# Kernel tuning notes

Measured on AMD Instinct MI355X. Metric: run time of the kernel, lower is better.

## Reference

```python
import jax, jax.numpy as jnp
import numpy as np

B, T, C, H, DH = 2, 2048, 768, 12, 64


def setup_inputs() -> dict:
    key = jax.random.key(0)
    k1, k2, k3 = jax.random.split(key, 3)
    x = jax.random.normal(k1, (B, T, C), dtype=jnp.float32)
    Wqkv = jax.random.normal(k2, (C, 3 * C), dtype=jnp.float32) * (C ** -0.5)
    Wout = jax.random.normal(k3, (C, C), dtype=jnp.float32) * (C ** -0.5)
    return {"x": x, "Wqkv": Wqkv, "Wout": Wout}


def reference(x, Wqkv, Wout):
    b, t, c = x.shape
    qkv = x @ Wqkv  # [B,T,3C]
    q, k, v = jnp.split(qkv, 3, axis=-1)
    # [B,T,C] -> [B,H,T,dh]
    q = q.reshape(b, t, H, DH).transpose(0, 2, 1, 3)
    k = k.reshape(b, t, H, DH).transpose(0, 2, 1, 3)
    v = v.reshape(b, t, H, DH).transpose(0, 2, 1, 3)
    scale = DH ** -0.5
    scores = jnp.einsum('bhqd,bhkd->bhqk', q, k) * scale  # [B,H,T,T]
    causal = jnp.tril(jnp.ones((t, t), dtype=bool))
    scores = jnp.where(causal, scores, -jnp.inf)
    weights = jax.nn.softmax(scores, axis=-1)
    # dropout p=0.0 -> identity
    out = jnp.einsum('bhqk,bhkd->bhqd', weights, v)  # [B,H,T,dh]
    out = out.transpose(0, 2, 1, 3).reshape(b, t, c)
    return out @ Wout
```

## Files before the change

kernel.cpp:

```cpp
#include <hip/hip_runtime.h>
#include <hip/hip_bf16.h>

#define Bn 2
#define Tn 2048
#define Cn 768
#define Hn 12
#define Dn 64
#define N3n 2304
#define Mn 4096

#define MASKVAL (-30000.f)
#define NITEMS 1152
#define DEFER_THR 64.f
#define L2E8 0.1803368801111204f

typedef unsigned short u16;
typedef __attribute__((ext_vector_type(8))) unsigned short ushort8_t;
typedef __attribute__((ext_vector_type(8))) short bf16x8;
typedef __attribute__((ext_vector_type(4))) float f32x4;
typedef __attribute__((ext_vector_type(2))) unsigned int uint2v;
typedef __attribute__((address_space(1))) unsigned int* gas1_t;
typedef __attribute__((address_space(3))) unsigned int* las3_t;

__device__ __forceinline__ float bf2f(u16 u) {
  union { unsigned int i; float f; } v; v.i = ((unsigned int)u) << 16; return v.f;
}
__device__ __forceinline__ u16 f2bf(float f) {
  union { float f; unsigned int i; } v; v.f = f;
  return (u16)((v.i + 0x7fffu + ((v.i >> 16) & 1u)) >> 16);
}

#define E(qt, s0, s1, ck) (((qt) << 24) | ((s0) << 16) | ((s1) << 8) | (ck))
__constant__ unsigned int SCHED[48] = {
    E(31, 0, 16, 0), E(31, 16, 32, 1), E(30, 0, 16, 0), E(15, 0, 16, 2),
    E(30, 16, 31, 1), E(29, 0, 15, 0), E(29, 15, 30, 1), E(28, 0, 15, 0), E(14, 0, 15, 2),
    E(28, 15, 29, 1), E(27, 0, 14, 0), E(27, 14, 28, 1), E(26, 0, 14, 0), E(13, 0, 14, 2),
    E(26, 14, 27, 1), E(25, 0, 13, 0), E(25, 13, 26, 1), E(24, 0, 13, 0), E(12, 0, 13, 2),
    E(24, 13, 25, 1), E(23, 0, 12, 0), E(23, 12, 24, 1), E(22, 0, 12, 0), E(11, 0, 12, 2),
    E(22, 12, 23, 1), E(21, 0, 11, 0), E(21, 11, 22, 1), E(20, 0, 11, 0), E(10, 0, 11, 2),
    E(20, 11, 21, 1), E(19, 0, 10, 0), E(19, 10, 20, 1), E(18, 0, 10, 0), E(9, 0, 10, 2),
    E(18, 10, 19, 1), E(17, 0, 9, 0), E(17, 9, 18, 1), E(16, 0, 9, 0), E(8, 0, 9, 2),
    E(16, 9, 17, 1), E(7, 0, 8, 2),
    E(6, 0, 7, 2), E(5, 0, 6, 2), E(4, 0, 5, 2), E(3, 0, 4, 2), E(2, 0, 3, 2),
    E(1, 0, 2, 2), E(0, 0, 1, 2)};

__global__ __launch_bounds__(256) void prep_kernel(const float* __restrict__ x,
                                                   const float* __restrict__ Wqkv,
                                                   const float* __restrict__ Wout,
                                                   u16* __restrict__ xb,
                                                   u16* __restrict__ WqkvT,
                                                   u16* __restrict__ WoutT,
                                                   int* __restrict__ counter) {
  __shared__ u16 t[32][33];
  const int bx = blockIdx.x;
  const int tid = threadIdx.x;
  if (bx < 3072) {
    if (bx == 0 && tid == 0) *counter = 0;
    const int i = (bx * 256 + tid) * 4;
    float4 v = *(const float4*)(x + i);
    ushort4 s;
    s.x = f2bf(v.x); s.y = f2bf(v.y); s.z = f2bf(v.z); s.w = f2bf(v.w);
    *(ushort4*)(xb + i) = s;
  } else {
    const int idx = bx - 3072;
    const int gx = idx % 96, gy = idx / 96;
    const bool isA = gx < (N3n / 32);
    const float* in = isA ? Wqkv : Wout;
    u16* out = isA ? WqkvT : WoutT;
    const int Cc = isA ? N3n : Cn;
    const int c0 = (isA ? gx : gx - N3n / 32) * 32;
    const int r0 = gy * 32;
    const int tx = tid & 31, ty = tid >> 5;
#pragma unroll
    for (int i = 0; i < 4; i++)
      t[ty * 4 + i][tx] = f2bf(in[(size_t)(r0 + ty * 4 + i) * Cc + c0 + tx]);
    __syncthreads();
#pragma unroll
    for (int i = 0; i < 4; i++)
      out[(size_t)(c0 + ty * 4 + i) * Cn + r0 + tx] = t[tx][ty * 4 + i];
  }
}

#define BK 64

template <int EPI>
__global__ __launch_bounds__(256) void mfma_gemm(const u16* __restrict__ A,
                                                 const u16* __restrict__ BT,
                                                 u16* __restrict__ Q,
                                                 u16* __restrict__ Kd,
                                                 u16* __restrict__ VT,
                                                 float* __restrict__ out) {
  __shared__ __align__(16) u16 Ash[128 * BK];
  __shared__ __align__(16) u16 Bsh[128 * BK];
  const int tid = threadIdx.x;
  const int wv = tid >> 6, lane = tid & 63;
  const int lo = lane & 15, quad = lane >> 4;
  const int wm = wv & 1, wn = wv >> 1;

  const int nwg = gridDim.x * gridDim.y;
  const int cpx = nwg >> 3;
  const int lid = blockIdx.y * gridDim.x + blockIdx.x;
  const int swz = (lid & 7) * cpx + (lid >> 3);
  const int n0 = (swz % gridDim.x) * 128;
  const int m0 = (swz / gridDim.x) * 128;

  const int srow = lane >> 3;
  const int scol = (lane & 7) << 3;

  f32x4 acc[4][4];
#pragma unroll
  for (int i = 0; i < 4; i++)
#pragma unroll
    for (int j = 0; j < 4; j++) acc[i][j] = f32x4{0.f, 0.f, 0.f, 0.f};

  for (int k0 = 0; k0 < Cn; k0 += BK) {
    __syncthreads();
#pragma unroll
    for (int c = 0; c < 4; c++) {
      const int rb = (wv << 5) + (c << 3);
      const int gr = rb + srow;
      __builtin_amdgcn_global_load_lds(
          (gas1_t)(A + (size_t)(m0 + gr) * Cn + k0 + scol),
          (las3_t)(&Ash[rb * BK]), 16, 0, 0);
      __builtin_amdgcn_global_load_lds(
          (gas1_t)(BT + (size_t)(n0 + gr) * Cn + k0 + scol),
          (las3_t)(&Bsh[rb * BK]), 16, 0, 0);
    }
    __syncthreads();

    bf16x8 af[4][2], bfr[4][2];
#pragma unroll
    for (int t = 0; t < 4; t++) {
#pragma unroll
      for (int s = 0; s < 2; s++) {
        af[t][s]  = *(const bf16x8*)&Ash[(wm * 64 + t * 16 + lo) * BK + s * 32 + (quad << 3)];
        bfr[t][s] = *(const bf16x8*)&Bsh[(wn * 64 + t * 16 + lo) * BK + s * 32 + (quad << 3)];
      }
    }
#pragma unroll
    for (int mt = 0; mt < 4; mt++)
#pragma unroll
      for (int nt = 0; nt < 4; nt++) {
        acc[mt][nt] = __builtin_amdgcn_mfma_f32_16x16x32_bf16(af[mt][0], bfr[nt][0],
                                                              acc[mt][nt], 0, 0, 0);
        acc[mt][nt] = __builtin_amdgcn_mfma_f32_16x16x32_bf16(af[mt][1], bfr[nt][1],
                                                              acc[mt][nt], 0, 0, 0);
      }
  }

  if (EPI == 0) {
    const int which = n0 / Cn;
    const int h = ((n0 % Cn) >> 6) + wn;
    const int bb = m0 >> 11;
    const int t_base = (m0 & (Tn - 1)) + wm * 64;
    if (which < 2) {
      u16* dst = ((which == 0) ? Q : Kd) + (size_t)(bb * Hn + h) * Tn * Dn;
#pragma unroll
      for (int mt = 0; mt < 4; mt++)
#pragma unroll
        for (int nt = 0; nt < 4; nt++)
#pragma unroll
          for (int r = 0; r < 4; r++) {
            const int t = t_base + mt * 16 + (quad << 2) + r;
            dst[(size_t)t * Dn + nt * 16 + lo] = f2bf(acc[mt][nt][r]);
          }
    } else {
      u16* dst = VT + (size_t)(bb * Hn + h) * Dn * Tn;
#pragma unroll
      for (int mt = 0; mt < 4; mt++)
#pragma unroll
        for (int nt = 0; nt < 4; nt++) {
          const int t = t_base + mt * 16 + (quad << 2);
          const int d = nt * 16 + lo;
          ushort4 st;
          st.x = f2bf(acc[mt][nt][0]); st.y = f2bf(acc[mt][nt][1]);
          st.z = f2bf(acc[mt][nt][2]); st.w = f2bf(acc[mt][nt][3]);
          *(ushort4*)&dst[(size_t)d * Tn + t] = st;
        }
    }
  } else {
#pragma unroll
    for (int mt = 0; mt < 4; mt++)
#pragma unroll
      for (int nt = 0; nt < 4; nt++)
#pragma unroll
        for (int r = 0; r < 4; r++) {
          const int m = m0 + wm * 64 + mt * 16 + (quad << 2) + r;
          out[(size_t)m * Cn + n0 + wn * 64 + nt * 16 + lo] = acc[mt][nt][r];
        }
  }
}

#define TILE_W (64 * 64)

__global__ __launch_bounds__(256) void attn_kernel(const u16* __restrict__ Q,
                                                   const u16* __restrict__ K,
                                                   const u16* __restrict__ VT,
                                                   u16* __restrict__ O,
                                                   int* __restrict__ counter,
                                                   float* __restrict__ po,
                                                   float* __restrict__ pm,
                                                   float* __restrict__ pl) {
  __shared__ __align__(16) u16 Ksh[2 * TILE_W];
  __shared__ __align__(16) u16 Vsh[2 * TILE_W];
  int* sip = (int*)&Ksh[TILE_W];

  const int tid = threadIdx.x;
  const int wv = tid >> 6, lane = tid & 63;
  const int lo = lane & 15, quad = lane >> 4;
  const int lo7 = lo & 7;
  const int ck0 = (quad ^ lo7) << 3;
  const int ck1 = ck0 ^ 32;
  const int sr = tid >> 3;
  const int sc = (tid & 7) << 3;
  const int scw = (((tid & 7) ^ (sr & 7)) << 3);
  const int t7 = tid & 7;
  const int vb0 = (((t7 & 6) ^ (sr & 7)) << 3) + ((t7 & 1) << 2);
  const int vb1 = ((((t7 & 6) | 1) ^ (sr & 7)) << 3) + ((t7 & 1) << 2);

  for (;;) {
    if (tid == 0) *sip = atomicAdd(counter, 1);
    __syncthreads();
    const int item = *sip;
    if (item >= NITEMS) return;

    const unsigned int e = SCHED[item / 24];
    const int qt = e >> 24, ck = e & 255;
    const int jstart = ((e >> 16) & 255) << 6;
    const int jend   = ((e >> 8) & 255) << 6;
    const int q0 = qt << 6;
    const int hb = item % 24;
    const int h = hb % 12, b = hb / 12;
    const size_t base = (size_t)(b * Hn + h) * Tn * Dn;
    const size_t vtb  = (size_t)(b * Hn + h) * Dn * Tn;

    const u16* qp = Q + base + (size_t)(q0 + (wv << 4) + lo) * Dn + (quad << 3);
    const bf16x8 aq0 = *(const bf16x8*)qp;
    const bf16x8 aq1 = *(const bf16x8*)(qp + 32);

    f32x4 o[4] = {f32x4{0,0,0,0}, f32x4{0,0,0,0}, f32x4{0,0,0,0}, f32x4{0,0,0,0}};
    float m1 = MASKVAL;
    float l1 = 0.f;

#pragma unroll
    for (int it = 0; it < 2; it++) {
      const int r = sr + it * 32;
      *(ushort8_t*)&Ksh[r * 64 + scw] =
          *(const ushort8_t*)(K + base + (size_t)(jstart + r) * Dn + sc);
      union { ushort8_t u; uint2v hh[2]; } vv;
      vv.u = *(const ushort8_t*)(VT + vtb + (size_t)r * Tn + jstart + sc);
      *(uint2v*)&Vsh[r * 64 + vb0] = vv.hh[0];
      *(uint2v*)&Vsh[r * 64 + vb1] = vv.hh[1];
    }
    __syncthreads();

    int cur = 0;
    const int qrel = (wv << 4) + lo;

    for (int j0 = jstart; j0 < jend; j0 += 64) {
      const bool hasnext = (j0 + 64 < jend);

      ushort8_t kr[2], vr[2];
      if (hasnext) {
#pragma unroll
        for (int it = 0; it < 2; it++) {
          const int r = sr + it * 32;
          kr[it] = *(const ushort8_t*)(K + base + (size_t)(j0 + 64 + r) * Dn + sc);
          vr[it] = *(const ushort8_t*)(VT + vtb + (size_t)r * Tn + j0 + 64 + sc);
        }
      }

      const u16* Kb_ = &Ksh[cur * TILE_W];
      const u16* Vb_ = &Vsh[cur * TILE_W];

      f32x4 s[4];
#pragma unroll
      for (int nt = 0; nt < 4; nt++) {
        const bf16x8 bk0 = *(const bf16x8*)(&Kb_[(nt * 16 + lo) * 64 + ck0]);
        const bf16x8 bk1 = *(const bf16x8*)(&Kb_[(nt * 16 + lo) * 64 + ck1]);
        f32x4 a = {0.f, 0.f, 0.f, 0.f};
        a = __builtin_amdgcn_mfma_f32_16x16x32_bf16(bk0, aq0, a, 0, 0, 0);
        a = __builtin_amdgcn_mfma_f32_16x16x32_bf16(bk1, aq1, a, 0, 0, 0);
        s[nt] = a;
      }

      if (j0 == q0) {
#pragma unroll
        for (int nt = 0; nt < 4; nt++)
#pragma unroll
          for (int r = 0; r < 4; r++) {
            const int kv = nt * 16 + (quad << 2) + r;
            if (kv > qrel) s[nt][r] = MASKVAL;
          }
      }

      float mx = fmaxf(s[0][0], s[0][1]);
      mx = fmaxf(fmaxf(mx, s[0][2]), s[0][3]);
      mx = fmaxf(fmaxf(mx, s[1][0]), s[1][1]);
      mx = fmaxf(fmaxf(mx, s[1][2]), s[1][3]);
      mx = fmaxf(fmaxf(mx, s[2][0]), s[2][1]);
      mx = fmaxf(fmaxf(mx, s[2][2]), s[2][3]);
      mx = fmaxf(fmaxf(mx, s[3][0]), s[3][1]);
      mx = fmaxf(fmaxf(mx, s[3][2]), s[3][3]);
      const float pmax = mx;

      if (!__all(pmax <= m1 + DEFER_THR)) {
        float mr = fmaxf(pmax, __shfl_xor(pmax, 16));
        mr = fmaxf(mr, __shfl_xor(mr, 32));
        const float mnew = fmaxf(m1, mr);
        const float alpha = __builtin_amdgcn_exp2f(L2E8 * (m1 - mnew));
        m1 = mnew;
        l1 *= alpha;
        float ar[4];
#pragma unroll
        for (int r = 0; r < 4; r++) ar[r] = __shfl(alpha, (quad << 2) + r);
#pragma unroll
        for (int nt = 0; nt < 4; nt++)
#pragma unroll
          for (int r = 0; r < 4; r++) o[nt][r] *= ar[r];
      }

      const float mb2 = L2E8 * m1;
      float sum = 0.f;
#pragma unroll
      for (int nt = 0; nt < 4; nt++)
#pragma unroll
        for (int r = 0; r < 4; r++) {
          const float p = __builtin_amdgcn_exp2f(L2E8 * s[nt][r] - mb2);
          s[nt][r] = p;
          sum += p;
        }
      l1 += sum;

      unsigned int A0, B0, A1, B1, A2, B2, A3, B3;
      asm("v_cvt_pk_bf16_f32 %0, %1, %2" : "=v"(A0) : "v"(s[0][0]), "v"(s[0][1]));
      asm("v_cvt_pk_bf16_f32 %0, %1, %2" : "=v"(B0) : "v"(s[0][2]), "v"(s[0][3]));
      asm("v_cvt_pk_bf16_f32 %0, %1, %2" : "=v"(A1) : "v"(s[1][0]), "v"(s[1][1]));
      asm("v_cvt_pk_bf16_f32 %0, %1, %2" : "=v"(B1) : "v"(s[1][2]), "v"(s[1][3]));
      asm("v_cvt_pk_bf16_f32 %0, %1, %2" : "=v"(A2) : "v"(s[2][0]), "v"(s[2][1]));
      asm("v_cvt_pk_bf16_f32 %0, %1, %2" : "=v"(B2) : "v"(s[2][2]), "v"(s[2][3]));
      asm("v_cvt_pk_bf16_f32 %0, %1, %2" : "=v"(A3) : "v"(s[3][0]), "v"(s[3][1]));
      asm("v_cvt_pk_bf16_f32 %0, %1, %2" : "=v"(B3) : "v"(s[3][2]), "v"(s[3][3]));
      const auto rA01 = __builtin_amdgcn_permlane32_swap(A0, A1, false, false);
      const auto rB01 = __builtin_amdgcn_permlane32_swap(B0, B1, false, false);
      const auto rA23 = __builtin_amdgcn_permlane32_swap(A2, A3, false, false);
      const auto rB23 = __builtin_amdgcn_permlane32_swap(B2, B3, false, false);
      union { unsigned int w[4]; bf16x8 v; } pa0u, pa1u;
      pa0u.w[0] = rA01[0]; pa0u.w[1] = rB01[0];
      pa0u.w[2] = rA01[1]; pa0u.w[3] = rB01[1];
      pa1u.w[0] = rA23[0]; pa1u.w[1] = rB23[0];
      pa1u.w[2] = rA23[1]; pa1u.w[3] = rB23[1];

#pragma unroll
      for (int nt = 0; nt < 4; nt++) {
        const bf16x8 bv0 = *(const bf16x8*)(&Vb_[(nt * 16 + lo) * 64 + ck0]);
        const bf16x8 bv1 = *(const bf16x8*)(&Vb_[(nt * 16 + lo) * 64 + ck1]);
        o[nt] = __builtin_amdgcn_mfma_f32_16x16x32_bf16(pa0u.v, bv0, o[nt], 0, 0, 0);
        o[nt] = __builtin_amdgcn_mfma_f32_16x16x32_bf16(pa1u.v, bv1, o[nt], 0, 0, 0);
      }

      if (hasnext) {
        const int nb = cur ^ 1;
#pragma unroll
        for (int it = 0; it < 2; it++) {
          const int r = sr + it * 32;
          *(ushort8_t*)&Ksh[nb * TILE_W + r * 64 + scw] = kr[it];
          union { ushort8_t u; uint2v hh[2]; } vv;
          vv.u = vr[it];
          *(uint2v*)&Vsh[nb * TILE_W + r * 64 + vb0] = vv.hh[0];
          *(uint2v*)&Vsh[nb * TILE_W + r * 64 + vb1] = vv.hh[1];
        }
      }
      __syncthreads();
      cur ^= 1;
    }

    float lt = l1;
    lt += __shfl_xor(lt, 16);
    lt += __shfl_xor(lt, 32);
    const float linv = 1.f / lt;
    float ir[4];
#pragma unroll
    for (int r = 0; r < 4; r++) ir[r] = __shfl(linv, (quad << 2) + r);

    if (ck == 2) {
#pragma unroll
      for (int nt = 0; nt < 4; nt++)
#pragma unroll
        for (int r = 0; r < 4; r++) {
          const int row = q0 + (wv << 4) + (quad << 2) + r;
          const int col = h * 64 + nt * 16 + lo;
          O[(size_t)(b * Tn + row) * Cn + col] = f2bf(o[nt][r] * ir[r]);
        }
    } else {
      const int st = hb * 16 + (qt - 16);
      const int pidx = st * 2 + ck;
      float* pO = po + ((size_t)pidx << 12);
#pragma unroll
      for (int nt = 0; nt < 4; nt++)
#pragma unroll
        for (int r = 0; r < 4; r++)
          pO[((wv << 4) + (quad << 2) + r) * 64 + nt * 16 + lo] = o[nt][r] * ir[r];
      if (quad == 0) {
        pm[pidx * 64 + (wv << 4) + lo] = m1;
        pl[pidx * 64 + (wv << 4) + lo] = lt;
      }
    }
  }
}

__global__ __launch_bounds__(256) void combine_kernel(const float* __restrict__ po,
                                                      const float* __restrict__ pm,
                                                      const float* __restrict__ pl,
                                                      u16* __restrict__ O) {
  const int st = blockIdx.x;
  const int hb = st >> 4;
  const int h = hb % 12, b = hb / 12;
  const int q0 = (16 + (st & 15)) << 6;
  const int tid = threadIdx.x;
  const int row = tid >> 2, cc0 = (tid & 3) << 4;
  const float* pa = po + (((size_t)st * 2) << 12) + row * 64 + cc0;
  const float* pb = pa + 4096;
  const float ma = pm[st * 128 + row],      la = pl[st * 128 + row];
  const float mb = pm[st * 128 + 64 + row], lb = pl[st * 128 + 64 + row];
  const float mm = fmaxf(ma, mb);
  float wa = la * __builtin_amdgcn_exp2f(L2E8 * (ma - mm));
  float wb = lb * __builtin_amdgcn_exp2f(L2E8 * (mb - mm));
  const float wi = 1.f / (wa + wb);
  wa *= wi; wb *= wi;
  u16* Orow = O + (size_t)(b * Tn + q0 + row) * Cn + h * 64 + cc0;
#pragma unroll
  for (int i = 0; i < 16; i += 4) {
    const float4 va = *(const float4*)(pa + i);
    const float4 vb = *(const float4*)(pb + i);
    ushort4 s4;
    s4.x = f2bf(wa * va.x + wb * vb.x);
    s4.y = f2bf(wa * va.y + wb * vb.y);
    s4.z = f2bf(wa * va.z + wb * vb.z);
    s4.w = f2bf(wa * va.w + wb * vb.w);
    *(ushort4*)(Orow + i) = s4;
  }
}

extern "C" void kernel_launch(void* const* d_in, const int* in_sizes, int n_in,
                              void* d_out, int out_size, void* d_ws, size_t ws_size,
                              hipStream_t stream) {
  const float* x    = (const float*)d_in[0];
  const float* Wqkv = (const float*)d_in[1];
  const float* Wout = (const float*)d_in[2];
  float* out = (float*)d_out;

  const size_t per = (size_t)Bn * Hn * Tn * Dn;
  u16* xb    = (u16*)d_ws;
  u16* WqkvT = xb + (size_t)Mn * Cn;
  u16* WoutT = WqkvT + (size_t)N3n * Cn;
  u16* Qb    = WoutT + (size_t)Cn * Cn;
  u16* Kb    = Qb + per;
  u16* VTb   = Kb + per;
  u16* attn  = VTb + per;
  int* counter = (int*)(attn + (size_t)Mn * Cn);
  float* po = (float*)(counter + 512);
  float* pm = po + (size_t)768 * 4096;
  float* pl = pm + (size_t)768 * 64;

  prep_kernel<<<dim3(3072 + 2304), 256, 0, stream>>>(x, Wqkv, Wout, xb, WqkvT,
                                                     WoutT, counter);
  mfma_gemm<0><<<dim3(N3n / 128, Mn / 128), 256, 0, stream>>>(xb, WqkvT, Qb, Kb, VTb, nullptr);
  attn_kernel<<<dim3(1024), 256, 0, stream>>>(Qb, Kb, VTb, attn, counter, po, pm, pl);
  combine_kernel<<<dim3(384), 256, 0, stream>>>(po, pm, pl, attn);
  mfma_gemm<1><<<dim3(Cn / 128, Mn / 128), 256, 0, stream>>>(attn, WoutT, nullptr, nullptr, nullptr, out);
}
```

Baseline: 181.6 us.

## Split work queue into per-XCD counters and tree-reduce softmax max/sum

Replaces the single global atomic work counter with eight counters indexed by blockIdx&7. Each group of blocks then takes items for a fixed set of three (batch, head) pairs, so K/V tiles stay local to one XCD's L2 and contention on the atomic is reduced. The row max and row sum in the softmax are also rewritten as balanced trees to shorten dependency chains. The risk is load imbalance, because each group drains its own queue independently and may finish at a different time.

```diff
diff --git a/kernel.cpp b/kernel.cpp
--- a/kernel.cpp
+++ b/kernel.cpp
@@ -10,7 +10,7 @@
 #define Mn 4096
 
 #define MASKVAL (-30000.f)
-#define NITEMS 1152
+#define NIT_G 144
 #define DEFER_THR 64.f
 #define L2E8 0.1803368801111204f
 
@@ -55,7 +55,7 @@
   const int bx = blockIdx.x;
   const int tid = threadIdx.x;
   if (bx < 3072) {
-    if (bx == 0 && tid == 0) *counter = 0;
+    if (bx == 0 && tid < 8) counter[tid] = 0;
     const int i = (bx * 256 + tid) * 4;
     float4 v = *(const float4*)(x + i);
     ushort4 s;
@@ -206,6 +206,7 @@
   int* sip = (int*)&Ksh[TILE_W];
 
   const int tid = threadIdx.x;
+  const int g = blockIdx.x & 7;
   const int wv = tid >> 6, lane = tid & 63;
   const int lo = lane & 15, quad = lane >> 4;
   const int lo7 = lo & 7;
@@ -219,17 +220,17 @@
   const int vb1 = ((((t7 & 6) | 1) ^ (sr & 7)) << 3) + ((t7 & 1) << 2);
 
   for (;;) {
-    if (tid == 0) *sip = atomicAdd(counter, 1);
+    if (tid == 0) *sip = atomicAdd(&counter[g], 1);
     __syncthreads();
-    const int item = *sip;
-    if (item >= NITEMS) return;
-
-    const unsigned int e = SCHED[item / 24];
+    const int il = *sip;
+    if (il >= NIT_G) return;
+
+    const unsigned int e = SCHED[il / 3];
     const int qt = e >> 24, ck = e & 255;
     const int jstart = ((e >> 16) & 255) << 6;
     const int jend   = ((e >> 8) & 255) << 6;
     const int q0 = qt << 6;
-    const int hb = item % 24;
+    const int hb = g * 3 + il % 3;
     const int h = hb % 12, b = hb / 12;
     const size_t base = (size_t)(b * Hn + h) * Tn * Dn;
     const size_t vtb  = (size_t)(b * Hn + h) * Dn * Tn;
@@ -294,15 +295,11 @@
           }
       }
 
-      float mx = fmaxf(s[0][0], s[0][1]);
-      mx = fmaxf(fmaxf(mx, s[0][2]), s[0][3]);
-      mx = fmaxf(fmaxf(mx, s[1][0]), s[1][1]);
-      mx = fmaxf(fmaxf(mx, s[1][2]), s[1][3]);
-      mx = fmaxf(fmaxf(mx, s[2][0]), s[2][1]);
-      mx = fmaxf(fmaxf(mx, s[2][2]), s[2][3]);
-      mx = fmaxf(fmaxf(mx, s[3][0]), s[3][1]);
-      mx = fmaxf(fmaxf(mx, s[3][2]), s[3][3]);
-      const float pmax = mx;
+      const float mxa = fmaxf(fmaxf(s[0][0], s[0][1]), fmaxf(s[0][2], s[0][3]));
+      const float mxb = fmaxf(fmaxf(s[1][0], s[1][1]), fmaxf(s[1][2], s[1][3]));
+      const float mxc = fmaxf(fmaxf(s[2][0], s[2][1]), fmaxf(s[2][2], s[2][3]));
+      const float mxd = fmaxf(fmaxf(s[3][0], s[3][1]), fmaxf(s[3][2], s[3][3]));
+      const float pmax = fmaxf(fmaxf(mxa, mxb), fmaxf(mxc, mxd));
 
       if (!__all(pmax <= m1 + DEFER_THR)) {
         float mr = fmaxf(pmax, __shfl_xor(pmax, 16));
@@ -321,16 +318,18 @@
       }
 
       const float mb2 = L2E8 * m1;
-      float sum = 0.f;
 #pragma unroll
       for (int nt = 0; nt < 4; nt++)
 #pragma unroll
-        for (int r = 0; r < 4; r++) {
-          const float p = __builtin_amdgcn_exp2f(L2E8 * s[nt][r] - mb2);
-          s[nt][r] = p;
-          sum += p;
-        }
-      l1 += sum;
+        for (int r = 0; r < 4; r++)
+          s[nt][r] = __builtin_amdgcn_exp2f(L2E8 * s[nt][r] - mb2);
+      {
+        const float s0 = (s[0][0] + s[0][1]) + (s[0][2] + s[0][3]);
+        const float s1 = (s[1][0] + s[1][1]) + (s[1][2] + s[1][3]);
+        const float s2 = (s[2][0] + s[2][1]) + (s[2][2] + s[2][3]);
+        const float s3 = (s[3][0] + s[3][1]) + (s[3][2] + s[3][3]);
+        l1 += (s0 + s1) + (s2 + s3);
+      }
 
       unsigned int A0, B0, A1, B1, A2, B2, A3, B3;
       asm("v_cvt_pk_bf16_f32 %0, %1, %2" : "=v"(A0) : "v"(s[0][0]), "v"(s[0][1]));
```

New measurement: 179.7 us. Within noise of the previous version (-1.0%).
